# Performance work log

Measured on AMD Instinct MI355X. Metric: run time of the kernel, lower is better.

The kernel has to match this reference:

```python
import jax, jax.numpy as jnp
import numpy as np

B, N, D = 2, 2048, 1024
H = 16
DH = D // H

def setup_inputs() -> dict:
    key = jax.random.key(0)
    ks = jax.random.split(key, 9)
    s = 1.0 / np.sqrt(D)
    return {
        "x": jax.random.normal(ks[0], (B, N, D), dtype=jnp.float32),
        "Wq": jax.random.uniform(ks[1], (D, D), jnp.float32, -s, s),
        "bq": jax.random.uniform(ks[2], (D,), jnp.float32, -s, s),
        "Wk": jax.random.uniform(ks[3], (D, D), jnp.float32, -s, s),
        "bk": jax.random.uniform(ks[4], (D,), jnp.float32, -s, s),
        "Wv": jax.random.uniform(ks[5], (D, D), jnp.float32, -s, s),
        "bv": jax.random.uniform(ks[6], (D,), jnp.float32, -s, s),
        "Wo": jax.random.uniform(ks[7], (D, D), jnp.float32, -s, s),
        "bo": jax.random.uniform(ks[8], (D,), jnp.float32, -s, s),
    }

def reference(x, Wq, bq, Wk, bk, Wv, bv, Wo, bo):
    # torch Linear: y = x @ W.T + b
    scale = 1.0 / np.sqrt(DH)
    q = (x @ Wq.T + bq).reshape(B, N, H, DH).transpose(0, 2, 1, 3)  # [B,H,N,DH]
    k = (x @ Wk.T + bk).reshape(B, N, H, DH).transpose(0, 2, 1, 3)
    v = (x @ Wv.T + bv).reshape(B, N, H, DH).transpose(0, 2, 1, 3)
    scores = jnp.einsum('bhnd,bhmd->bhnm', q, k) * scale  # [B,H,N,N]
    attn = jax.nn.softmax(scores, axis=-1)
    out = jnp.einsum('bhnm,bhmd->bhnd', attn, v)  # [B,H,N,DH]
    out = out.transpose(0, 2, 1, 3).reshape(B, N, D)
    return out @ Wo.T + bo
```

## Files before the change

### kernel.cpp

```cpp
#include <hip/hip_runtime.h>
#include <hip/hip_bf16.h>

#define B_  2
#define N_  2048
#define D_  1024
#define H_  16
#define DH_ 64
#define BN_ (B_*N_)

typedef __attribute__((ext_vector_type(8))) short short8;
typedef __attribute__((ext_vector_type(4))) float f32x4;
typedef __attribute__((ext_vector_type(16))) float f32x16;
typedef __attribute__((ext_vector_type(4))) unsigned int uint4v;

typedef __attribute__((address_space(3))) unsigned int lds_u32_t;
typedef const __attribute__((address_space(1))) unsigned int glb_u32_t;

__device__ __forceinline__ void async_load16(const unsigned short* g, unsigned short* l) {
    __builtin_amdgcn_global_load_lds((glb_u32_t*)g, (lds_u32_t*)l, 16, 0, 0);
}

__device__ __forceinline__ unsigned short f2bf(float f) {
    __hip_bfloat16 h = __float2bfloat16(f);
    return *reinterpret_cast<unsigned short*>(&h);
}

__device__ __forceinline__ unsigned int pkbf(float a, float b) {
    unsigned int ua = __float_as_uint(a) + 0x8000u;
    unsigned int ub = __float_as_uint(b) + 0x8000u;
    return __builtin_amdgcn_perm(ub, ua, 0x07060302);
}

#if __has_builtin(__builtin_amdgcn_exp2f)
#define EXP2(x) __builtin_amdgcn_exp2f(x)
#else
#define EXP2(x) exp2f(x)
#endif

#define QSCL 0.1803368801111204f

__global__ __launch_bounds__(256) void cast_kernel(
    const float* __restrict__ x,  const float* __restrict__ wq,
    const float* __restrict__ wk, const float* __restrict__ wv,
    const float* __restrict__ wo,
    unsigned short* __restrict__ xb,  unsigned short* __restrict__ wqb,
    unsigned short* __restrict__ wkb, unsigned short* __restrict__ wvb,
    unsigned short* __restrict__ wob)
{
    const size_t NX = (size_t)BN_ * D_;
    const size_t NW = (size_t)D_ * D_;
    size_t i = ((size_t)blockIdx.x * 256 + threadIdx.x) * 4;
    const float* src; unsigned short* dst; size_t off;
    if (i < NX) { src = x; dst = xb; off = i; }
    else {
        size_t j = (i - NX) >> 20;
        off = (i - NX) & (NW - 1);
        src = (j == 0) ? wq : (j == 1) ? wk : (j == 2) ? wv : wo;
        dst = (j == 0) ? wqb : (j == 1) ? wkb : (j == 2) ? wvb : wob;
    }
    float4 v = *(const float4*)(src + off);
    ushort4 o;
    o.x = f2bf(v.x); o.y = f2bf(v.y); o.z = f2bf(v.z); o.w = f2bf(v.w);
    *(ushort4*)(dst + off) = o;
}

template<int OUT_MODE>
__device__ __forceinline__ void gemm_body(
    unsigned short* __restrict__ As, unsigned short* __restrict__ Bs,
    const unsigned short* __restrict__ A, const unsigned short* __restrict__ W,
    const float* __restrict__ bias, void* __restrict__ Cout, int bx, int by)
{
    constexpr int K = D_;
    const int tid  = threadIdx.x;
    const int lane = tid & 63;
    const int wave = tid >> 6;
    const int l15 = lane & 15, quad = lane >> 4;

    f32x4 acc[4][2] = {};
    const int row0 = by * 64, col0 = bx * 128;

    const int srow = lane >> 3;
    const int scb  = lane & 7;

    for (int k0 = 0; k0 < K; k0 += 64) {
        __syncthreads();
#pragma unroll
        for (int cc = 0; cc < 2; ++cc) {
            int c  = wave * 2 + cc;
            int lr = c * 8 + srow;
            int gcol = k0 + ((scb ^ (lr & 7)) * 8);
            async_load16(A + (size_t)(row0 + lr) * K + gcol, As + c * 512);
        }
#pragma unroll
        for (int cc = 0; cc < 4; ++cc) {
            int c  = wave * 4 + cc;
            int lr = c * 8 + srow;
            int gcol = k0 + ((scb ^ (lr & 7)) * 8);
            async_load16(W + (size_t)(col0 + lr) * K + gcol, Bs + c * 512);
        }
        __syncthreads();

#pragma unroll
        for (int kf = 0; kf < 2; ++kf) {
            const int swz = ((kf * 4 + quad) ^ (l15 & 7)) * 8;
            short8 af[4], bf[2];
#pragma unroll
            for (int mi = 0; mi < 4; mi++)
                af[mi] = *(const short8*)(&As[(mi * 16 + l15) * 64 + swz]);
#pragma unroll
            for (int ni = 0; ni < 2; ni++)
                bf[ni] = *(const short8*)(&Bs[(wave * 32 + ni * 16 + l15) * 64 + swz]);
#pragma unroll
            for (int mi = 0; mi < 4; mi++)
#pragma unroll
                for (int ni = 0; ni < 2; ni++)
                    acc[mi][ni] = __builtin_amdgcn_mfma_f32_16x16x32_bf16(
                        af[mi], bf[ni], acc[mi][ni], 0, 0, 0);
        }
    }

    if (OUT_MODE == 2) {
        __syncthreads();
#pragma unroll
        for (int ni = 0; ni < 2; ni++) {
            int c = wave * 32 + ni * 16 + l15;
            float bv = bias[col0 + c];
#pragma unroll
            for (int mi = 0; mi < 4; mi++) {
                int r = mi * 16 + quad * 4;
                ushort4 pk;
                pk.x = f2bf(acc[mi][ni][0] + bv);
                pk.y = f2bf(acc[mi][ni][1] + bv);
                pk.z = f2bf(acc[mi][ni][2] + bv);
                pk.w = f2bf(acc[mi][ni][3] + bv);
                *(ushort4*)(Bs + c * 64 + (r ^ ((c & 7) << 3))) = pk;
            }
        }
        __syncthreads();
#pragma unroll
        for (int itx = 0; itx < 4; ++itx) {
            int item = itx * 256 + tid;
            int c  = item >> 3;
            int rb = item & 7;
            uint4v v = *(const uint4v*)(Bs + c * 64 + ((rb ^ (c & 7)) * 8));
            *(uint4v*)((unsigned short*)Cout + (size_t)(col0 + c) * BN_ + row0 + rb * 8) = v;
        }
        return;
    }

    if (OUT_MODE == 1 || OUT_MODE == 3) {
        __syncthreads();
#pragma unroll
        for (int ni = 0; ni < 2; ni++) {
            int c = wave * 32 + ni * 16 + l15;
            float bv = bias[col0 + c];
#pragma unroll
            for (int mi = 0; mi < 4; mi++) {
#pragma unroll
                for (int r = 0; r < 4; r++) {
                    float v = acc[mi][ni][r] + bv;
                    if (OUT_MODE == 3) v *= QSCL;
                    int row = mi * 16 + quad * 4 + r;
                    Bs[row * 128 + (c ^ ((row & 7) << 3))] = f2bf(v);
                }
            }
        }
        __syncthreads();
#pragma unroll
        for (int itx = 0; itx < 4; ++itx) {
            int item = itx * 256 + tid;
            int row = item >> 4;
            int cb  = item & 15;
            uint4v v = *(const uint4v*)(Bs + row * 128 + ((cb ^ (row & 7)) * 8));
            *(uint4v*)((unsigned short*)Cout + (size_t)(row0 + row) * D_ + col0 + cb * 8) = v;
        }
        return;
    }

#pragma unroll
    for (int ni = 0; ni < 2; ni++) {
        int col = col0 + wave * 32 + ni * 16 + l15;
        float bv = bias[col];
#pragma unroll
        for (int mi = 0; mi < 4; mi++) {
            int row = row0 + mi * 16 + quad * 4;
#pragma unroll
            for (int r = 0; r < 4; r++)
                ((float*)Cout)[(size_t)(row + r) * D_ + col] = acc[mi][ni][r] + bv;
        }
    }
}

__device__ __forceinline__ void xcd_swz(int& bx, int& by) {
    int w = blockIdx.y * 8 + blockIdx.x;
    int s = (w & 7) * 64 + (w >> 3);
    bx = s & 7; by = s >> 3;
}

__global__ __launch_bounds__(256, 5) void qkv_gemm(
    const unsigned short* __restrict__ xb,
    const unsigned short* __restrict__ wqb, const unsigned short* __restrict__ wkb,
    const unsigned short* __restrict__ wvb,
    const float* __restrict__ bq, const float* __restrict__ bk, const float* __restrict__ bv,
    unsigned short* __restrict__ q, unsigned short* __restrict__ k, unsigned short* __restrict__ vt)
{
    __shared__ __align__(16) unsigned short As[64 * 64];
    __shared__ __align__(16) unsigned short Bs[128 * 64];
    int bx, by; xcd_swz(bx, by);
    if (blockIdx.z == 0)
        gemm_body<3>(As, Bs, xb, wqb, bq, q,  bx, by);
    else if (blockIdx.z == 1)
        gemm_body<1>(As, Bs, xb, wkb, bk, k,  bx, by);
    else
        gemm_body<2>(As, Bs, xb, wvb, bv, vt, bx, by);
}

__global__ __launch_bounds__(256, 5) void out_gemm(
    const unsigned short* __restrict__ attn, const unsigned short* __restrict__ wob,
    const float* __restrict__ bo, float* __restrict__ out)
{
    __shared__ __align__(16) unsigned short As[64 * 64];
    __shared__ __align__(16) unsigned short Bs[128 * 64];
    int bx, by; xcd_swz(bx, by);
    gemm_body<0>(As, Bs, attn, wob, bo, out, bx, by);
}

__global__ __launch_bounds__(256) void attn_kernel(
    const unsigned short* __restrict__ q, const unsigned short* __restrict__ k,
    const unsigned short* __restrict__ vt, unsigned short* __restrict__ o)
{
    __shared__ __align__(16) unsigned short Ks[2][64 * 64];
    __shared__ __align__(16) unsigned short Vs[2][64 * 64];

    const int tid = threadIdx.x;
    const int lane = tid & 63, wave = tid >> 6;
    const int l31 = lane & 31, kq = lane >> 5;
    const int bh = blockIdx.x;
    const int qt = blockIdx.y;
    const int b = bh >> 4, h = bh & 15;

    const unsigned short* qb = q  + (size_t)b * N_ * D_ + h * DH_;
    const unsigned short* kb = k  + (size_t)b * N_ * D_ + h * DH_;
    const unsigned short* vb = vt + (size_t)h * DH_ * BN_ + (size_t)b * N_;

    const int qrow0 = qt * 128 + wave * 32;

    short8 qf[4];
#pragma unroll
    for (int s = 0; s < 4; s++)
        qf[s] = *(const short8*)(qb + (size_t)(qrow0 + l31) * D_ + s * 16 + kq * 8);

    f32x16 oacc[2] = {};
    float lsum = 0.f;

    const int srow = lane >> 3, scb = lane & 7;

    auto stage = [&](int bi, int kv0) {
#pragma unroll
        for (int cc = 0; cc < 2; ++cc) {
            int c  = wave * 2 + cc;
            int lr = c * 8 + srow;
            int swz8 = (scb ^ (lr & 7)) * 8;
            async_load16(kb + (size_t)(kv0 + lr) * D_ + swz8, (unsigned short*)Ks[bi] + c * 512);
            async_load16(vb + (size_t)lr * BN_ + kv0 + swz8,  (unsigned short*)Vs[bi] + c * 512);
        }
    };

    stage(0, 0);

    const int NIT = N_ / 64;
    for (int it = 0; it < NIT; ++it) {
        const int cur = it & 1;
        __syncthreads();
        if (it + 1 < NIT) stage(cur ^ 1, (it + 1) * 64);

        const unsigned short* Kc = Ks[cur];
        const unsigned short* Vc = Vs[cur];

        f32x16 st[2] = {};
        __builtin_amdgcn_s_setprio(1);
#pragma unroll
        for (int s = 0; s < 4; s++) {
#pragma unroll
            for (int mb = 0; mb < 2; mb++) {
                short8 kfr = *(const short8*)((const char*)Kc +
                    (mb * 32 + l31) * 128 + (((2 * s + kq) ^ (l31 & 7)) * 16));
                st[mb] = __builtin_amdgcn_mfma_f32_32x32x16_bf16(
                    kfr, qf[s], st[mb], 0, 0, 0);
            }
        }
        __builtin_amdgcn_s_setprio(0);

#pragma unroll
        for (int mb = 0; mb < 2; mb++) {
            unsigned int pk[8];
#pragma unroll
            for (int g = 0; g < 4; g++) {
                float p0 = EXP2(st[mb][g * 4 + 0]);
                float p1 = EXP2(st[mb][g * 4 + 1]);
                float p2 = EXP2(st[mb][g * 4 + 2]);
                float p3 = EXP2(st[mb][g * 4 + 3]);
                lsum += (p0 + p1) + (p2 + p3);
                pk[2 * g + 0] = pkbf(p0, p1);
                pk[2 * g + 1] = pkbf(p2, p3);
            }
            __builtin_amdgcn_s_setprio(1);
#pragma unroll
            for (int s = 0; s < 2; s++) {
                uint4v fu;
                fu[0] = pk[4 * s + 0]; fu[1] = pk[4 * s + 1];
                fu[2] = pk[4 * s + 2]; fu[3] = pk[4 * s + 3];
                short8 pf = __builtin_bit_cast(short8, fu);
                const int blkA = 4 * mb + 2 * s;
#pragma unroll
                for (int nb = 0; nb < 2; nb++) {
                    const char* vrow = (const char*)Vc + (nb * 32 + l31) * 128;
                    uint2 vlo = *(const uint2*)(vrow + ((blkA       ^ (l31 & 7)) * 16) + kq * 8);
                    uint2 vhi = *(const uint2*)(vrow + (((blkA + 1) ^ (l31 & 7)) * 16) + kq * 8);
                    uint4v vu; vu[0] = vlo.x; vu[1] = vlo.y; vu[2] = vhi.x; vu[3] = vhi.y;
                    short8 vf = __builtin_bit_cast(short8, vu);
                    oacc[nb] = __builtin_amdgcn_mfma_f32_32x32x16_bf16(
                        pf, vf, oacc[nb], 0, 0, 0);
                }
            }
            __builtin_amdgcn_s_setprio(0);
        }
    }

    lsum += __shfl_xor(lsum, 32);
    __syncthreads();
    float* Lt = (float*)&Ks[0][0] + wave * 32;
    if (kq == 0) Lt[l31] = lsum;
    asm volatile("s_waitcnt lgkmcnt(0)" ::: "memory");

#pragma unroll
    for (int g = 0; g < 4; g++)
#pragma unroll
        for (int rr = 0; rr < 4; rr++) {
            int reg = g * 4 + rr;
            float inv = 1.f / Lt[rr + 8 * g + 4 * kq];
            int row = qrow0 + rr + 8 * g + 4 * kq;
            size_t base = ((size_t)b * N_ + row) * D_ + h * DH_;
#pragma unroll
            for (int nb = 0; nb < 2; nb++)
                o[base + nb * 32 + l31] = f2bf(oacc[nb][reg] * inv);
        }
}

extern "C" void kernel_launch(void* const* d_in, const int* in_sizes, int n_in,
                              void* d_out, int out_size, void* d_ws, size_t ws_size,
                              hipStream_t stream)
{
    const float* x  = (const float*)d_in[0];
    const float* Wq = (const float*)d_in[1];
    const float* bq = (const float*)d_in[2];
    const float* Wk = (const float*)d_in[3];
    const float* bk = (const float*)d_in[4];
    const float* Wv = (const float*)d_in[5];
    const float* bv = (const float*)d_in[6];
    const float* Wo = (const float*)d_in[7];
    const float* bo = (const float*)d_in[8];
    float* out = (float*)d_out;

    char* ws = (char*)d_ws;
    unsigned short* xb  = (unsigned short*)(ws + 0);
    unsigned short* wqb = (unsigned short*)(ws + 8388608);
    unsigned short* wkb = (unsigned short*)(ws + 10485760);
    unsigned short* wvb = (unsigned short*)(ws + 12582912);
    unsigned short* wob = (unsigned short*)(ws + 14680064);
    unsigned short* qd  = (unsigned short*)(ws + 16777216);
    unsigned short* kd  = (unsigned short*)(ws + 25165824);
    unsigned short* vtd = (unsigned short*)(ws + 33554432);
    unsigned short* ad  = (unsigned short*)(ws + 41943040);

    cast_kernel<<<8192, 256, 0, stream>>>(x, Wq, Wk, Wv, Wo, xb, wqb, wkb, wvb, wob);
    qkv_gemm<<<dim3(8, 64, 3), 256, 0, stream>>>(xb, wqb, wkb, wvb, bq, bk, bv, qd, kd, vtd);
    attn_kernel<<<dim3(32, 16), 256, 0, stream>>>(qd, kd, vtd, ad);
    out_gemm<<<dim3(8, 64), 256, 0, stream>>>(ad, wob, bo, out);
}
```

Baseline: 194.9 us.

## Fuse Q/K/V projections into one GEMM kernel sharing the x tile

Result: no change. 191.2 us (-1.9%).

```diff
diff --git a/kernel.cpp b/kernel.cpp
--- a/kernel.cpp
+++ b/kernel.cpp
@@ -64,6 +64,114 @@
     *(ushort4*)(dst + off) = o;
 }
 
+__global__ __launch_bounds__(256, 2) void qkv_fused(
+    const unsigned short* __restrict__ xb,
+    const unsigned short* __restrict__ wqb, const unsigned short* __restrict__ wkb,
+    const unsigned short* __restrict__ wvb,
+    const float* __restrict__ bq, const float* __restrict__ bk, const float* __restrict__ bv,
+    unsigned short* __restrict__ q, unsigned short* __restrict__ k, unsigned short* __restrict__ vt)
+{
+    __shared__ __align__(16) unsigned short As[64 * 64];
+    __shared__ __align__(16) unsigned short Bq[128 * 64];
+    __shared__ __align__(16) unsigned short Bk[128 * 64];
+    __shared__ __align__(16) unsigned short Bv[128 * 64];
+
+    const int tid  = threadIdx.x;
+    const int lane = tid & 63;
+    const int wave = tid >> 6;
+    const int l15 = lane & 15, quad = lane >> 4;
+
+    const int p  = blockIdx.x & 3, hh = blockIdx.x >> 2;
+    const int bx = p * 2 + (blockIdx.y & 1);
+    const int by = hh * 32 + (blockIdx.y >> 1);
+    const int row0 = by * 64, col0 = bx * 128;
+
+    const int srow = lane >> 3, scb = lane & 7;
+
+    f32x4 aq[4][2] = {}, ak[4][2] = {}, av[4][2] = {};
+
+    for (int k0 = 0; k0 < D_; k0 += 64) {
+        __syncthreads();
+#pragma unroll
+        for (int cc = 0; cc < 2; ++cc) {
+            int c  = wave * 2 + cc;
+            int lr = c * 8 + srow;
+            int gcol = k0 + ((scb ^ (lr & 7)) * 8);
+            async_load16(xb + (size_t)(row0 + lr) * D_ + gcol, As + c * 512);
+        }
+#pragma unroll
+        for (int cc = 0; cc < 4; ++cc) {
+            int c  = wave * 4 + cc;
+            int lr = c * 8 + srow;
+            int gcol = k0 + ((scb ^ (lr & 7)) * 8);
+            size_t off = (size_t)(col0 + lr) * D_ + gcol;
+            async_load16(wqb + off, Bq + c * 512);
+            async_load16(wkb + off, Bk + c * 512);
+            async_load16(wvb + off, Bv + c * 512);
+        }
+        __syncthreads();
+
+#pragma unroll
+        for (int kf = 0; kf < 2; ++kf) {
+            const int swz = ((kf * 4 + quad) ^ (l15 & 7)) * 8;
+            short8 af[4];
+#pragma unroll
+            for (int mi = 0; mi < 4; mi++)
+                af[mi] = *(const short8*)(&As[(mi * 16 + l15) * 64 + swz]);
+#pragma unroll
+            for (int ni = 0; ni < 2; ni++) {
+                const int boff = (wave * 32 + ni * 16 + l15) * 64 + swz;
+                short8 fq = *(const short8*)(&Bq[boff]);
+                short8 fk = *(const short8*)(&Bk[boff]);
+                short8 fv = *(const short8*)(&Bv[boff]);
+#pragma unroll
+                for (int mi = 0; mi < 4; mi++) {
+                    aq[mi][ni] = __builtin_amdgcn_mfma_f32_16x16x32_bf16(af[mi], fq, aq[mi][ni], 0, 0, 0);
+                    ak[mi][ni] = __builtin_amdgcn_mfma_f32_16x16x32_bf16(af[mi], fk, ak[mi][ni], 0, 0, 0);
+                    av[mi][ni] = __builtin_amdgcn_mfma_f32_16x16x32_bf16(af[mi], fv, av[mi][ni], 0, 0, 0);
+                }
+            }
+        }
+    }
+
+    __syncthreads();
+#pragma unroll
+    for (int ni = 0; ni < 2; ni++) {
+        int c = wave * 32 + ni * 16 + l15;
+        float biq = bq[col0 + c], bik = bk[col0 + c], biv = bv[col0 + c];
+#pragma unroll
+        for (int mi = 0; mi < 4; mi++) {
+            int r4 = mi * 16 + quad * 4;
+            ushort4 pv;
+            pv.x = f2bf(av[mi][ni][0] + biv);
+            pv.y = f2bf(av[mi][ni][1] + biv);
+            pv.z = f2bf(av[mi][ni][2] + biv);
+            pv.w = f2bf(av[mi][ni][3] + biv);
+            *(ushort4*)(Bv + c * 64 + (r4 ^ ((c & 7) << 3))) = pv;
+#pragma unroll
+            for (int r = 0; r < 4; r++) {
+                int row = r4 + r;
+                int sc  = c ^ ((row & 7) << 3);
+                Bq[row * 128 + sc] = f2bf((aq[mi][ni][r] + biq) * QSCL);
+                Bk[row * 128 + sc] = f2bf(ak[mi][ni][r] + bik);
+            }
+        }
+    }
+    __syncthreads();
+#pragma unroll
+    for (int itx = 0; itx < 4; ++itx) {
+        int item = itx * 256 + tid;
+        int row = item >> 4, cb = item & 15;
+        uint4v vq = *(const uint4v*)(Bq + row * 128 + ((cb ^ (row & 7)) * 8));
+        *(uint4v*)(q + (size_t)(row0 + row) * D_ + col0 + cb * 8) = vq;
+        uint4v vk = *(const uint4v*)(Bk + row * 128 + ((cb ^ (row & 7)) * 8));
+        *(uint4v*)(k + (size_t)(row0 + row) * D_ + col0 + cb * 8) = vk;
+        int c = item >> 3, rb = item & 7;
+        uint4v vv = *(const uint4v*)(Bv + c * 64 + ((rb ^ (c & 7)) * 8));
+        *(uint4v*)(vt + (size_t)(col0 + c) * BN_ + row0 + rb * 8) = vv;
+    }
+}
+
 template<int OUT_MODE>
 __device__ __forceinline__ void gemm_body(
     unsigned short* __restrict__ As, unsigned short* __restrict__ Bs,
@@ -119,74 +227,16 @@
         }
     }
 
-    if (OUT_MODE == 2) {
-        __syncthreads();
-#pragma unroll
-        for (int ni = 0; ni < 2; ni++) {
-            int c = wave * 32 + ni * 16 + l15;
-            float bv = bias[col0 + c];
-#pragma unroll
-            for (int mi = 0; mi < 4; mi++) {
-                int r = mi * 16 + quad * 4;
-                ushort4 pk;
-                pk.x = f2bf(acc[mi][ni][0] + bv);
-                pk.y = f2bf(acc[mi][ni][1] + bv);
-                pk.z = f2bf(acc[mi][ni][2] + bv);
-                pk.w = f2bf(acc[mi][ni][3] + bv);
-                *(ushort4*)(Bs + c * 64 + (r ^ ((c & 7) << 3))) = pk;
-            }
-        }
-        __syncthreads();
-#pragma unroll
-        for (int itx = 0; itx < 4; ++itx) {
-            int item = itx * 256 + tid;
-            int c  = item >> 3;
-            int rb = item & 7;
-            uint4v v = *(const uint4v*)(Bs + c * 64 + ((rb ^ (c & 7)) * 8));
-            *(uint4v*)((unsigned short*)Cout + (size_t)(col0 + c) * BN_ + row0 + rb * 8) = v;
-        }
-        return;
-    }
-
-    if (OUT_MODE == 1 || OUT_MODE == 3) {
-        __syncthreads();
-#pragma unroll
-        for (int ni = 0; ni < 2; ni++) {
-            int c = wave * 32 + ni * 16 + l15;
-            float bv = bias[col0 + c];
-#pragma unroll
-            for (int mi = 0; mi < 4; mi++) {
-#pragma unroll
-                for (int r = 0; r < 4; r++) {
-                    float v = acc[mi][ni][r] + bv;
-                    if (OUT_MODE == 3) v *= QSCL;
-                    int row = mi * 16 + quad * 4 + r;
-                    Bs[row * 128 + (c ^ ((row & 7) << 3))] = f2bf(v);
-                }
-            }
-        }
-        __syncthreads();
-#pragma unroll
-        for (int itx = 0; itx < 4; ++itx) {
-            int item = itx * 256 + tid;
-            int row = item >> 4;
-            int cb  = item & 15;
-            uint4v v = *(const uint4v*)(Bs + row * 128 + ((cb ^ (row & 7)) * 8));
-            *(uint4v*)((unsigned short*)Cout + (size_t)(row0 + row) * D_ + col0 + cb * 8) = v;
-        }
-        return;
-    }
-
 #pragma unroll
     for (int ni = 0; ni < 2; ni++) {
         int col = col0 + wave * 32 + ni * 16 + l15;
-        float bv = bias[col];
+        float bvv = bias[col];
 #pragma unroll
         for (int mi = 0; mi < 4; mi++) {
             int row = row0 + mi * 16 + quad * 4;
 #pragma unroll
             for (int r = 0; r < 4; r++)
-                ((float*)Cout)[(size_t)(row + r) * D_ + col] = acc[mi][ni][r] + bv;
+                ((float*)Cout)[(size_t)(row + r) * D_ + col] = acc[mi][ni][r] + bvv;
         }
     }
 }
@@ -195,24 +245,6 @@
     int w = blockIdx.y * 8 + blockIdx.x;
     int s = (w & 7) * 64 + (w >> 3);
     bx = s & 7; by = s >> 3;
-}
-
-__global__ __launch_bounds__(256, 5) void qkv_gemm(
-    const unsigned short* __restrict__ xb,
-    const unsigned short* __restrict__ wqb, const unsigned short* __restrict__ wkb,
-    const unsigned short* __restrict__ wvb,
-    const float* __restrict__ bq, const float* __restrict__ bk, const float* __restrict__ bv,
-    unsigned short* __restrict__ q, unsigned short* __restrict__ k, unsigned short* __restrict__ vt)
-{
-    __shared__ __align__(16) unsigned short As[64 * 64];
-    __shared__ __align__(16) unsigned short Bs[128 * 64];
-    int bx, by; xcd_swz(bx, by);
-    if (blockIdx.z == 0)
-        gemm_body<3>(As, Bs, xb, wqb, bq, q,  bx, by);
-    else if (blockIdx.z == 1)
-        gemm_body<1>(As, Bs, xb, wkb, bk, k,  bx, by);
-    else
-        gemm_body<2>(As, Bs, xb, wvb, bv, vt, bx, by);
 }
 
 __global__ __launch_bounds__(256, 5) void out_gemm(
@@ -374,7 +406,7 @@
     unsigned short* ad  = (unsigned short*)(ws + 41943040);
 
     cast_kernel<<<8192, 256, 0, stream>>>(x, Wq, Wk, Wv, Wo, xb, wqb, wkb, wvb, wob);
-    qkv_gemm<<<dim3(8, 64, 3), 256, 0, stream>>>(xb, wqb, wkb, wvb, bq, bk, bv, qd, kd, vtd);
+    qkv_fused<<<dim3(8, 64), 256, 0, stream>>>(xb, wqb, wkb, wvb, bq, bk, bv, qd, kd, vtd);
     attn_kernel<<<dim3(32, 16), 256, 0, stream>>>(qd, kd, vtd, ad);
     out_gemm<<<dim3(8, 64), 256, 0, stream>>>(ad, wob, bo, out);
 }
```
